# Kernel tuning notes

Measured on AMD Instinct MI355X. Metric: run time of the kernel, lower is better.

The kernel has to match this reference:

```python
import jax, jax.numpy as jnp
import numpy as np

GAMMA = 0.1
ENERGY = 0.5
BATCH = 64
INF = 1e10  # finite 'infinity' so exp(-INF/gamma) underflows to exactly 0


def softdtw_batch(D, gamma):
    """Batched soft-DTW over pairwise frame-distance matrices.
    D: [P, T, T] squared-Euclidean distances. Returns R(T-1,T-1): [P].
    DP is parallelized across anti-diagonals (wavefront)."""
    P, T, _ = D.shape
    iarr = jnp.arange(T)

    def body(carry, k):
        Rm2, Rm1 = carry  # diagonals k-2 and k-1, each [P, T] indexed by row i
        j = k - iarr
        valid = (j >= 0) & (j < T)
        d = D[:, iarr, jnp.clip(j, 0, T - 1)]  # [P, T]
        pad = jnp.full((P, 1), INF, D.dtype)
        r_up = jnp.concatenate([pad, Rm1[:, :-1]], axis=1)      # R(i-1, j)
        r_left = Rm1                                            # R(i, j-1)
        corner = jnp.where(k == 0, jnp.float32(0.0), jnp.float32(INF))
        r_diag = jnp.concatenate([jnp.full((P, 1), 1.0, D.dtype) * corner,
                                  Rm2[:, :-1]], axis=1)         # R(i-1, j-1)
        z = jnp.stack([r_up, r_left, r_diag], axis=0)           # [3, P, T]
        smin = -gamma * jax.nn.logsumexp(-z / gamma, axis=0)
        Rk = jnp.where(valid[None, :], d + smin, INF)
        return (Rm1, Rk), None

    init = (jnp.full((P, T), INF, D.dtype), jnp.full((P, T), INF, D.dtype))
    (_, Rlast), _ = jax.lax.scan(body, init, jnp.arange(2 * T - 1))
    return Rlast[:, T - 1]


def setup_inputs() -> dict:
    key = jax.random.key(0)
    k1, k2 = jax.random.split(key)
    xxx = jax.random.normal(k1, (BATCH, 64, 13), dtype=jnp.float32)
    yyy = jax.random.normal(k2, (BATCH, 64, 13), dtype=jnp.float32)
    return {"xxx": xxx, "yyy": yyy}


def reference(xxx, yyy):
    B = BATCH
    full = jnp.concatenate([xxx, yyy], axis=0)  # [N, T, d]
    N, T, _ = full.shape
    # pairwise squared-Euclidean frame distances: [N, N, T, T]
    sq = jnp.sum(full * full, axis=-1)                      # [N, T]
    dots = jnp.einsum('aid,bjd->abij', full, full)          # [N, N, T, T]
    D = sq[:, None, :, None] + sq[None, :, None, :] - 2.0 * dots
    R = softdtw_batch(D.reshape(N * N, T, T), GAMMA)        # [N*N]
    sim = R.reshape(N, N)
    eye = jnp.eye(N, dtype=bool)
    sim = jnp.where(eye, 0.0, sim)  # i==j pairs skipped in original (left as 0)
    sim = sim / ENERGY
    pos = jnp.diagonal(sim, offset=B)                       # [B]
    positives = jnp.concatenate([pos, pos], axis=0)         # [2B] (source uses +B offset twice)
    loss = jnp.mean(-positives + jax.nn.logsumexp(sim, axis=-1))
    return loss
```

## Files before the change

### kernel.cpp

```cpp
#include <hip/hip_runtime.h>

#define TT 64
#define DIM 13
#define NSEQ 128
#define NWAVE 2080
#define NSTEP (TT + 16 - 1)
#define INFV 1e10f
#define C_EXP 14.4269504088896f
#define C_INV 0.06931471805599453f

typedef _Float16 h2 __attribute__((ext_vector_type(2)));

__device__ __forceinline__ float fdot2(h2 a, h2 b, float c) {
    return __builtin_amdgcn_fdot2(a, b, c, false);
}
__device__ __forceinline__ h2 mkh2(float a, float b) {
    h2 p; p.x = (_Float16)a; p.y = (_Float16)b; return p;
}
__device__ __forceinline__ h2 bch2(unsigned u) { return __builtin_bit_cast(h2, u); }
__device__ __forceinline__ float rowshr1_inf(float x) {
    int r = __builtin_amdgcn_update_dpp(__builtin_bit_cast(int, INFV),
                                        __builtin_bit_cast(int, x),
                                        0x111, 0xf, 0xf, false);
    return __builtin_bit_cast(float, r);
}
__device__ __forceinline__ float smstep(float S, float lf, float dg, float acc) {
    float m  = fminf(fminf(S, lf), dg);
    float md = __builtin_amdgcn_fmed3f(S, lf, dg);
    float M  = fmaxf(fmaxf(S, lf), dg);
    float s  = 1.0f + __builtin_amdgcn_exp2f(m - md) + __builtin_amdgcn_exp2f(m - M);
    return fmaf(acc, C_EXP, m - __builtin_amdgcn_logf(s));
}
__device__ __forceinline__ int Tq4(int N) {
    int q = N >> 2, r = N & 3;
    return 2 * q * (q + 1) + r * (q + 1);
}

__global__ __launch_bounds__(256, 2) void sdtw_pairs(const float* __restrict__ xxx,
                                                     const float* __restrict__ yyy,
                                                     float* __restrict__ simR) {
    __shared__ unsigned xl[4][7 * TT];
    const int wave = threadIdx.x >> 6;
    const int lane = threadIdx.x & 63;
    const int quarter = lane >> 4;
    const int sj = lane & 15;
    const int t = blockIdx.x * 4 + wave;

    int a = 127 - (int)sqrtf(8.0f * (float)(NWAVE - t));
    if (a < 0) a = 0;
    if (a > 126) a = 126;
    while (NWAVE - Tq4(127 - a) > t) a--;
    while (a < 126 && NWAVE - Tq4(127 - (a + 1)) <= t) a++;
    const int q = t - (NWAVE - Tq4(127 - a));
    const int b0 = a + 1 + 4 * q;
    const int b = (b0 + quarter < 128) ? b0 + quarter : 127;
    h2 yA[7], yB[7], yC[7], yD[7];
    float sqA = 0.f, sqB = 0.f, sqC = 0.f, sqD = 0.f;
    {
        const float* fb = ((b < 64) ? xxx + (size_t)b * TT * DIM
                                    : yyy + (size_t)(b - 64) * TT * DIM) + (4 * sj) * DIM;
        float vA[DIM], vB[DIM], vC[DIM], vD[DIM];
#pragma unroll
        for (int c = 0; c < DIM; c++) {
            vA[c] = fb[c];            sqA += vA[c] * vA[c];
            vB[c] = fb[DIM + c];      sqB += vB[c] * vB[c];
            vC[c] = fb[2 * DIM + c];  sqC += vC[c] * vC[c];
            vD[c] = fb[3 * DIM + c];  sqD += vD[c] * vD[c];
        }
#pragma unroll
        for (int c = 0; c < 6; c++) {
            yA[c] = mkh2(vA[2 * c], vA[2 * c + 1]);
            yB[c] = mkh2(vB[2 * c], vB[2 * c + 1]);
            yC[c] = mkh2(vC[2 * c], vC[2 * c + 1]);
            yD[c] = mkh2(vD[2 * c], vD[2 * c + 1]);
        }
        yA[6] = mkh2(vA[12], 1.0f);
        yB[6] = mkh2(vB[12], 1.0f);
        yC[6] = mkh2(vC[12], 1.0f);
        yD[6] = mkh2(vD[12], 1.0f);
    }

    {
        const float* fx = ((a < 64) ? xxx + (size_t)a * TT * DIM
                                    : yyy + (size_t)(a - 64) * TT * DIM) + lane * DIM;
        float xv[DIM], sqx = 0.f;
#pragma unroll
        for (int c = 0; c < DIM; c++) { xv[c] = fx[c]; sqx += xv[c] * xv[c]; }
        unsigned* dst = &xl[wave][lane];
#pragma unroll
        for (int c = 0; c < 6; c++)
            dst[c * TT] = __builtin_bit_cast(unsigned, mkh2(-2.f * xv[2 * c], -2.f * xv[2 * c + 1]));
        dst[6 * TT] = __builtin_bit_cast(unsigned, mkh2(-2.f * xv[12], sqx));
    }
    __syncthreads();

    const unsigned* xp = xl[wave];
    float SA = INFV, SB = INFV, SC = INFV, SD = INFV;
    float dgA = (sj == 0) ? 0.f : INFV;
    int ic = (-sj) & (TT - 1);

#pragma unroll 2
    for (int k = 0; k < NSTEP; k++) {
        unsigned w0 = xp[ic];
        unsigned w1 = xp[ic + 1 * TT];
        unsigned w2 = xp[ic + 2 * TT];
        unsigned w3 = xp[ic + 3 * TT];
        unsigned w4 = xp[ic + 4 * TT];
        unsigned w5 = xp[ic + 5 * TT];
        unsigned w6 = xp[ic + 6 * TT];
        ic = (ic + 1) & (TT - 1);

        float aA = sqA, aB = sqB, aC = sqC, aD = sqD;
        aA = fdot2(yA[0], bch2(w0), aA); aB = fdot2(yB[0], bch2(w0), aB);
        aC = fdot2(yC[0], bch2(w0), aC); aD = fdot2(yD[0], bch2(w0), aD);
        aA = fdot2(yA[1], bch2(w1), aA); aB = fdot2(yB[1], bch2(w1), aB);
        aC = fdot2(yC[1], bch2(w1), aC); aD = fdot2(yD[1], bch2(w1), aD);
        aA = fdot2(yA[2], bch2(w2), aA); aB = fdot2(yB[2], bch2(w2), aB);
        aC = fdot2(yC[2], bch2(w2), aC); aD = fdot2(yD[2], bch2(w2), aD);
        aA = fdot2(yA[3], bch2(w3), aA); aB = fdot2(yB[3], bch2(w3), aB);
        aC = fdot2(yC[3], bch2(w3), aC); aD = fdot2(yD[3], bch2(w3), aD);
        aA = fdot2(yA[4], bch2(w4), aA); aB = fdot2(yB[4], bch2(w4), aB);
        aC = fdot2(yC[4], bch2(w4), aC); aD = fdot2(yD[4], bch2(w4), aD);
        aA = fdot2(yA[5], bch2(w5), aA); aB = fdot2(yB[5], bch2(w5), aB);
        aC = fdot2(yC[5], bch2(w5), aC); aD = fdot2(yD[5], bch2(w5), aD);
        aA = fdot2(yA[6], bch2(w6), aA); aB = fdot2(yB[6], bch2(w6), aB);
        aC = fdot2(yC[6], bch2(w6), aC); aD = fdot2(yD[6], bch2(w6), aD);

        float lfA = rowshr1_inf(SD);

        float oA = SA; SA = smstep(SA, lfA, dgA, aA);
        float oB = SB; SB = smstep(SB, SA, oA, aB);
        float oC = SC; SC = smstep(SC, SB, oB, aC);
        SD = smstep(SD, SC, oC, aD);
        dgA = lfA;
    }

    if (sj == 15) {
        const float r = SD * C_INV;
        simR[a * NSEQ + b] = r;
        simR[b * NSEQ + a] = r;
    }
}

__global__ void row_lse(float* __restrict__ simR) {
    const int r = blockIdx.x;
    const int lane = threadIdx.x;
    const float* rowp = simR + r * NSEQ;
    float v0 = (lane == r) ? 0.f : 2.f * rowp[lane];
    const int c1 = lane + 64;
    float v1 = (c1 == r) ? 0.f : 2.f * rowp[c1];
    float mx = fmaxf(v0, v1);
#pragma unroll
    for (int o = 32; o; o >>= 1) mx = fmaxf(mx, __shfl_xor(mx, o));
    float s = __builtin_amdgcn_exp2f((v0 - mx) * 1.4426950408889634f)
            + __builtin_amdgcn_exp2f((v1 - mx) * 1.4426950408889634f);
#pragma unroll
    for (int o = 32; o; o >>= 1) s += __shfl_xor(s, o);
    if (lane == 0) {
        const int i = r & 63;
        float pos = 2.f * simR[i * NSEQ + i + 64];
        simR[r * NSEQ + r] = mx + 0.6931471805599453f * __builtin_amdgcn_logf(s) - pos;
    }
}

__global__ void final_loss(const float* __restrict__ simR, float* __restrict__ out) {
    __shared__ float red[NSEQ];
    const int tid = threadIdx.x;
    red[tid] = simR[tid * NSEQ + tid];
    __syncthreads();
    if (tid == 0) {
        float tsum = 0.f;
        for (int c = 0; c < NSEQ; c++) tsum += red[c];
        out[0] = tsum / (float)NSEQ;
    }
}

extern "C" void kernel_launch(void* const* d_in, const int* in_sizes, int n_in,
                              void* d_out, int out_size, void* d_ws, size_t ws_size,
                              hipStream_t stream) {
    const float* xxx = (const float*)d_in[0];
    const float* yyy = (const float*)d_in[1];
    float* out = (float*)d_out;
    float* simR = (float*)d_ws;

    sdtw_pairs<<<NWAVE / 4, 256, 0, stream>>>(xxx, yyy, simR);
    row_lse<<<NSEQ, 64, 0, stream>>>(simR);
    final_loss<<<1, NSEQ, 0, stream>>>(simR, out);
}
```

Baseline: 49.33 us.

## Interleave two pairs per 32-lane half with 2 columns per lane

Each 32-lane half-wave now runs two independent soft-DTW pairs, each with 2 columns per lane, instead of each 16-lane quarter running one pair with 4 columns per lane. The longer wavefront (95 steps instead of 79) is traded for a shorter per-step dependency chain and two independent chains that can interleave to hide exp/log latency. It uses a wave-wide DPP shift with explicit column-0 masking, and drops the min-blocks launch bound, which may change register allocation and occupancy.

```diff
diff --git a/kernel.cpp b/kernel.cpp
--- a/kernel.cpp
+++ b/kernel.cpp
@@ -4,7 +4,7 @@
 #define DIM 13
 #define NSEQ 128
 #define NWAVE 2080
-#define NSTEP (TT + 16 - 1)
+#define NSTEP (TT + 32 - 1)
 #define INFV 1e10f
 #define C_EXP 14.4269504088896f
 #define C_INV 0.06931471805599453f
@@ -18,10 +18,10 @@
     h2 p; p.x = (_Float16)a; p.y = (_Float16)b; return p;
 }
 __device__ __forceinline__ h2 bch2(unsigned u) { return __builtin_bit_cast(h2, u); }
-__device__ __forceinline__ float rowshr1_inf(float x) {
+__device__ __forceinline__ float shr1_inf(float x) {
     int r = __builtin_amdgcn_update_dpp(__builtin_bit_cast(int, INFV),
                                         __builtin_bit_cast(int, x),
-                                        0x111, 0xf, 0xf, false);
+                                        0x138, 0xf, 0xf, false);
     return __builtin_bit_cast(float, r);
 }
 __device__ __forceinline__ float smstep(float S, float lf, float dg, float acc) {
@@ -36,14 +36,14 @@
     return 2 * q * (q + 1) + r * (q + 1);
 }
 
-__global__ __launch_bounds__(256, 2) void sdtw_pairs(const float* __restrict__ xxx,
-                                                     const float* __restrict__ yyy,
-                                                     float* __restrict__ simR) {
+__global__ __launch_bounds__(256) void sdtw_pairs(const float* __restrict__ xxx,
+                                                  const float* __restrict__ yyy,
+                                                  float* __restrict__ simR) {
     __shared__ unsigned xl[4][7 * TT];
     const int wave = threadIdx.x >> 6;
     const int lane = threadIdx.x & 63;
-    const int quarter = lane >> 4;
-    const int sj = lane & 15;
+    const int hw = lane >> 5;
+    const int sj = lane & 31;
     const int t = blockIdx.x * 4 + wave;
 
     int a = 127 - (int)sqrtf(8.0f * (float)(NWAVE - t));
@@ -53,31 +53,35 @@
     while (a < 126 && NWAVE - Tq4(127 - (a + 1)) <= t) a++;
     const int q = t - (NWAVE - Tq4(127 - a));
     const int b0 = a + 1 + 4 * q;
-    const int b = (b0 + quarter < 128) ? b0 + quarter : 127;
-    h2 yA[7], yB[7], yC[7], yD[7];
-    float sqA = 0.f, sqB = 0.f, sqC = 0.f, sqD = 0.f;
+    const int b1 = (b0 + 2 * hw     < 128) ? b0 + 2 * hw     : 127;
+    const int b2 = (b0 + 2 * hw + 1 < 128) ? b0 + 2 * hw + 1 : 127;
+
+    h2 y1A[7], y1B[7], y2A[7], y2B[7];
+    float sq1A = 0.f, sq1B = 0.f, sq2A = 0.f, sq2B = 0.f;
     {
-        const float* fb = ((b < 64) ? xxx + (size_t)b * TT * DIM
-                                    : yyy + (size_t)(b - 64) * TT * DIM) + (4 * sj) * DIM;
+        const float* f1 = ((b1 < 64) ? xxx + (size_t)b1 * TT * DIM
+                                     : yyy + (size_t)(b1 - 64) * TT * DIM) + (2 * sj) * DIM;
+        const float* f2 = ((b2 < 64) ? xxx + (size_t)b2 * TT * DIM
+                                     : yyy + (size_t)(b2 - 64) * TT * DIM) + (2 * sj) * DIM;
         float vA[DIM], vB[DIM], vC[DIM], vD[DIM];
 #pragma unroll
         for (int c = 0; c < DIM; c++) {
-            vA[c] = fb[c];            sqA += vA[c] * vA[c];
-            vB[c] = fb[DIM + c];      sqB += vB[c] * vB[c];
-            vC[c] = fb[2 * DIM + c];  sqC += vC[c] * vC[c];
-            vD[c] = fb[3 * DIM + c];  sqD += vD[c] * vD[c];
+            vA[c] = f1[c];        sq1A += vA[c] * vA[c];
+            vB[c] = f1[DIM + c];  sq1B += vB[c] * vB[c];
+            vC[c] = f2[c];        sq2A += vC[c] * vC[c];
+            vD[c] = f2[DIM + c];  sq2B += vD[c] * vD[c];
         }
 #pragma unroll
         for (int c = 0; c < 6; c++) {
-            yA[c] = mkh2(vA[2 * c], vA[2 * c + 1]);
-            yB[c] = mkh2(vB[2 * c], vB[2 * c + 1]);
-            yC[c] = mkh2(vC[2 * c], vC[2 * c + 1]);
-            yD[c] = mkh2(vD[2 * c], vD[2 * c + 1]);
+            y1A[c] = mkh2(vA[2 * c], vA[2 * c + 1]);
+            y1B[c] = mkh2(vB[2 * c], vB[2 * c + 1]);
+            y2A[c] = mkh2(vC[2 * c], vC[2 * c + 1]);
+            y2B[c] = mkh2(vD[2 * c], vD[2 * c + 1]);
         }
-        yA[6] = mkh2(vA[12], 1.0f);
-        yB[6] = mkh2(vB[12], 1.0f);
-        yC[6] = mkh2(vC[12], 1.0f);
-        yD[6] = mkh2(vD[12], 1.0f);
+        y1A[6] = mkh2(vA[12], 1.0f);
+        y1B[6] = mkh2(vB[12], 1.0f);
+        y2A[6] = mkh2(vC[12], 1.0f);
+        y2B[6] = mkh2(vD[12], 1.0f);
     }
 
     {
@@ -95,8 +99,10 @@
     __syncthreads();
 
     const unsigned* xp = xl[wave];
-    float SA = INFV, SB = INFV, SC = INFV, SD = INFV;
-    float dgA = (sj == 0) ? 0.f : INFV;
+    float S1A = INFV, S1B = INFV, S2A = INFV, S2B = INFV;
+    float dg1 = (sj == 0) ? 0.f : INFV;
+    float dg2 = dg1;
+    const bool col0 = (sj == 0);
     int ic = (-sj) & (TT - 1);
 
 #pragma unroll 2
@@ -110,35 +116,43 @@
         unsigned w6 = xp[ic + 6 * TT];
         ic = (ic + 1) & (TT - 1);
 
-        float aA = sqA, aB = sqB, aC = sqC, aD = sqD;
-        aA = fdot2(yA[0], bch2(w0), aA); aB = fdot2(yB[0], bch2(w0), aB);
-        aC = fdot2(yC[0], bch2(w0), aC); aD = fdot2(yD[0], bch2(w0), aD);
-        aA = fdot2(yA[1], bch2(w1), aA); aB = fdot2(yB[1], bch2(w1), aB);
-        aC = fdot2(yC[1], bch2(w1), aC); aD = fdot2(yD[1], bch2(w1), aD);
-        aA = fdot2(yA[2], bch2(w2), aA); aB = fdot2(yB[2], bch2(w2), aB);
-        aC = fdot2(yC[2], bch2(w2), aC); aD = fdot2(yD[2], bch2(w2), aD);
-        aA = fdot2(yA[3], bch2(w3), aA); aB = fdot2(yB[3], bch2(w3), aB);
-        aC = fdot2(yC[3], bch2(w3), aC); aD = fdot2(yD[3], bch2(w3), aD);
-        aA = fdot2(yA[4], bch2(w4), aA); aB = fdot2(yB[4], bch2(w4), aB);
-        aC = fdot2(yC[4], bch2(w4), aC); aD = fdot2(yD[4], bch2(w4), aD);
-        aA = fdot2(yA[5], bch2(w5), aA); aB = fdot2(yB[5], bch2(w5), aB);
-        aC = fdot2(yC[5], bch2(w5), aC); aD = fdot2(yD[5], bch2(w5), aD);
-        aA = fdot2(yA[6], bch2(w6), aA); aB = fdot2(yB[6], bch2(w6), aB);
-        aC = fdot2(yC[6], bch2(w6), aC); aD = fdot2(yD[6], bch2(w6), aD);
-
-        float lfA = rowshr1_inf(SD);
-
-        float oA = SA; SA = smstep(SA, lfA, dgA, aA);
-        float oB = SB; SB = smstep(SB, SA, oA, aB);
-        float oC = SC; SC = smstep(SC, SB, oB, aC);
-        SD = smstep(SD, SC, oC, aD);
-        dgA = lfA;
-    }
-
-    if (sj == 15) {
-        const float r = SD * C_INV;
-        simR[a * NSEQ + b] = r;
-        simR[b * NSEQ + a] = r;
+        float a1A = sq1A, a1B = sq1B, a2A = sq2A, a2B = sq2B;
+        a1A = fdot2(y1A[0], bch2(w0), a1A); a1B = fdot2(y1B[0], bch2(w0), a1B);
+        a2A = fdot2(y2A[0], bch2(w0), a2A); a2B = fdot2(y2B[0], bch2(w0), a2B);
+        a1A = fdot2(y1A[1], bch2(w1), a1A); a1B = fdot2(y1B[1], bch2(w1), a1B);
+        a2A = fdot2(y2A[1], bch2(w1), a2A); a2B = fdot2(y2B[1], bch2(w1), a2B);
+        a1A = fdot2(y1A[2], bch2(w2), a1A); a1B = fdot2(y1B[2], bch2(w2), a1B);
+        a2A = fdot2(y2A[2], bch2(w2), a2A); a2B = fdot2(y2B[2], bch2(w2), a2B);
+        a1A = fdot2(y1A[3], bch2(w3), a1A); a1B = fdot2(y1B[3], bch2(w3), a1B);
+        a2A = fdot2(y2A[3], bch2(w3), a2A); a2B = fdot2(y2B[3], bch2(w3), a2B);
+        a1A = fdot2(y1A[4], bch2(w4), a1A); a1B = fdot2(y1B[4], bch2(w4), a1B);
+        a2A = fdot2(y2A[4], bch2(w4), a2A); a2B = fdot2(y2B[4], bch2(w4), a2B);
+        a1A = fdot2(y1A[5], bch2(w5), a1A); a1B = fdot2(y1B[5], bch2(w5), a1B);
+        a2A = fdot2(y2A[5], bch2(w5), a2A); a2B = fdot2(y2B[5], bch2(w5), a2B);
+        a1A = fdot2(y1A[6], bch2(w6), a1A); a1B = fdot2(y1B[6], bch2(w6), a1B);
+        a2A = fdot2(y2A[6], bch2(w6), a2A); a2B = fdot2(y2B[6], bch2(w6), a2B);
+
+        float lf1 = shr1_inf(S1B);
+        float lf2 = shr1_inf(S2B);
+        lf1 = col0 ? INFV : lf1;
+        lf2 = col0 ? INFV : lf2;
+
+        float o1 = S1A;
+        S1A = smstep(S1A, lf1, dg1, a1A);
+        S1B = smstep(S1B, S1A, o1, a1B);
+        dg1 = lf1;
+
+        float o2 = S2A;
+        S2A = smstep(S2A, lf2, dg2, a2A);
+        S2B = smstep(S2B, S2A, o2, a2B);
+        dg2 = lf2;
+    }
+
+    if (sj == 31) {
+        const float r1 = S1B * C_INV;
+        const float r2 = S2B * C_INV;
+        simR[a * NSEQ + b1] = r1; simR[b1 * NSEQ + a] = r1;
+        simR[a * NSEQ + b2] = r2; simR[b2 * NSEQ + a] = r2;
     }
 }
 
```

Result: slower. 56.68 us (+14.9%).
